# Kernel tuning notes

Measured on AMD Instinct MI355X. Metric: run time of the kernel, lower is better.

Reference implementation:

```python
import jax, jax.numpy as jnp
import numpy as np

D_MODEL = 2048
N_HEADS = 16
N_KV_HEADS = 2
HEAD_DIM = D_MODEL // N_HEADS  # 128
N_REP = N_HEADS // N_KV_HEADS  # 8
SCALE = HEAD_DIM ** -0.5


def setup_inputs() -> dict:
    key = jax.random.key(0)
    ks = jax.random.split(key, 5)
    B, N = 2, 2048
    x = jax.random.normal(ks[0], (B, N, D_MODEL), dtype=jnp.float32)
    # weights stored as [in, out] (math identical to torch Linear x @ W.T)
    s = D_MODEL ** -0.5
    Wq = jax.random.normal(ks[1], (D_MODEL, D_MODEL), dtype=jnp.float32) * s
    Wk = jax.random.normal(ks[2], (D_MODEL, N_KV_HEADS * HEAD_DIM), dtype=jnp.float32) * s
    Wv = jax.random.normal(ks[3], (D_MODEL, N_KV_HEADS * HEAD_DIM), dtype=jnp.float32) * s
    Wo = jax.random.normal(ks[4], (D_MODEL, D_MODEL), dtype=jnp.float32) * s
    return {"x": x, "Wq": Wq, "Wk": Wk, "Wv": Wv, "Wo": Wo}


def reference(x, Wq, Wk, Wv, Wo):
    B, N, C = x.shape
    q = (x @ Wq).reshape(B, N, N_HEADS, HEAD_DIM).transpose(0, 2, 1, 3)      # [B,H,N,hd]
    k = (x @ Wk).reshape(B, N, N_KV_HEADS, HEAD_DIM).transpose(0, 2, 1, 3)   # [B,Hkv,N,hd]
    v = (x @ Wv).reshape(B, N, N_KV_HEADS, HEAD_DIM).transpose(0, 2, 1, 3)
    if N_REP > 1:
        k = jnp.repeat(k, N_REP, axis=1)  # [B,H,N,hd]
        v = jnp.repeat(v, N_REP, axis=1)
    attn = jnp.einsum('bhnd,bhmd->bhnm', q, k) * SCALE
    attn = jax.nn.softmax(attn, axis=-1)
    out = jnp.einsum('bhnm,bhmd->bhnd', attn, v)
    out = out.transpose(0, 2, 1, 3).reshape(B, N, C)
    return out @ Wo
```

## Files before the change

kernel.cpp:

```cpp
#include <hip/hip_runtime.h>

typedef unsigned short u16;
typedef __attribute__((ext_vector_type(4))) float floatx4;
typedef __attribute__((ext_vector_type(2))) float floatx2;
typedef __attribute__((ext_vector_type(8))) __bf16 bf16x8;
typedef __attribute__((ext_vector_type(8))) u16 u16x8;

#define D_MODEL 2048
#define SEQ     2048
#define NH      16
#define NKV     2
#define HD      128
#define QKVN    2560
#define SCALE   0.08838834764831845f
#define QSCALE  (0.08838834764831845f * 1.4426950408889634f)
#define M_STATIC 20.0f

__device__ __forceinline__ u16 f2bf(float f) {
    unsigned int x = __float_as_uint(f);
    return (u16)((x + 0x7fffu + ((x >> 16) & 1u)) >> 16);
}

__device__ __forceinline__ void gload16(const u16* g, u16* l) {
    __builtin_amdgcn_global_load_lds((const __attribute__((address_space(1))) void*)g,
                                     (__attribute__((address_space(3))) void*)l, 16, 0, 0);
}

__global__ void f2b_k(const float* __restrict__ src, u16* __restrict__ dst, long n)
{
    long i = ((long)blockIdx.x * blockDim.x + threadIdx.x) * 8;
    if (i >= n) return;
    float4 a = *(const float4*)(src + i);
    float4 b = *(const float4*)(src + i + 4);
    u16x8 o;
    o[0] = f2bf(a.x); o[1] = f2bf(a.y); o[2] = f2bf(a.z); o[3] = f2bf(a.w);
    o[4] = f2bf(b.x); o[5] = f2bf(b.y); o[6] = f2bf(b.z); o[7] = f2bf(b.w);
    *(u16x8*)(dst + i) = o;
}

struct TrJob { const float* src; u16* dst; int ncol; float scale; };

__global__ void trw_k(TrJob j0, TrJob j1, TrJob j2, TrJob j3)
{
    TrJob j = (blockIdx.z == 0) ? j0 : (blockIdx.z == 1) ? j1
            : (blockIdx.z == 2) ? j2 : j3;
    int c0 = blockIdx.x * 64, r0 = blockIdx.y * 64;
    if (c0 >= j.ncol) return;
    __shared__ float tile[64][65];
    int tx = threadIdx.x, ty = threadIdx.y;
#pragma unroll
    for (int i = 0; i < 8; ++i) {
        int row = ty + i * 8;
        floatx2 v = *(const floatx2*)(j.src + (long)(r0 + row) * j.ncol + c0 + tx * 2);
        tile[row][tx * 2]     = v[0];
        tile[row][tx * 2 + 1] = v[1];
    }
    __syncthreads();
#pragma unroll
    for (int i = 0; i < 8; ++i) {
        int cc = ty + i * 8;
        unsigned int p = (unsigned int)f2bf(tile[tx * 2][cc] * j.scale)
                       | ((unsigned int)f2bf(tile[tx * 2 + 1][cc] * j.scale) << 16);
        *(unsigned int*)(j.dst + (long)(c0 + cc) * 2048 + r0 + tx * 2) = p;
    }
}

__global__ void trv_k(const u16* __restrict__ src, u16* __restrict__ dst)
{
    int b = blockIdx.z;
    const u16* s = src + (long)b * SEQ * QKVN;
    u16* d = dst + (long)b * 256 * 2048;
    int c0 = blockIdx.x * 64, r0 = blockIdx.y * 64;
    __shared__ u16 tile[64][66];
    int tx = threadIdx.x, ty = threadIdx.y;
#pragma unroll
    for (int i = 0; i < 8; ++i) {
        int row = ty + i * 8;
        unsigned int v = *(const unsigned int*)(s + (long)(r0 + row) * QKVN + c0 + tx * 2);
        *(unsigned int*)&tile[row][tx * 2] = v;
    }
    __syncthreads();
#pragma unroll
    for (int i = 0; i < 8; ++i) {
        int cc = ty + i * 8;
        unsigned int p = (unsigned int)tile[tx * 2][cc]
                       | ((unsigned int)tile[tx * 2 + 1][cc] << 16);
        *(unsigned int*)(d + (long)(c0 + cc) * 2048 + r0 + tx * 2) = p;
    }
}

template <bool F32OUT>
__global__ __launch_bounds__(256, 2) void gemm_bt_k(
    const u16* __restrict__ A, const u16* __restrict__ Bt, void* __restrict__ Cv,
    int K, int lda, int ldb, int ldc)
{
    __shared__ __align__(16) u16 As[128 * 64];
    __shared__ __align__(16) u16 Bs[128 * 64];
    const int tid  = threadIdx.x;
    const int wave = tid >> 6, lane = tid & 63;
    const int quad = lane >> 4, l16 = lane & 15;
    const long bm = (long)blockIdx.x * 128;
    const long bn = (long)blockIdx.y * 128;
    const int wr = (wave >> 1) * 64;
    const int wc = (wave & 1) * 64;

    floatx4 acc[4][4] = {};

    for (long k0 = 0; k0 < K; k0 += 64) {
#pragma unroll
        for (int t = 0; t < 4; ++t) {
            int c = tid + t * 256;
            int row = c >> 3, sl = c & 7;
            int kc = sl ^ (row & 7);
            gload16(A + (bm + row) * lda + k0 + kc * 8,
                    As + ((tid & ~63) + t * 256) * 8);
        }
#pragma unroll
        for (int t = 0; t < 4; ++t) {
            int c = tid + t * 256;
            int row = c >> 3, sl = c & 7;
            int kc = sl ^ (row & 7);
            gload16(Bt + (bn + row) * ldb + k0 + kc * 8,
                    Bs + ((tid & ~63) + t * 256) * 8);
        }
        __syncthreads();

#pragma unroll
        for (int ks = 0; ks < 2; ++ks) {
            bf16x8 af[4], bfr[4];
#pragma unroll
            for (int mt = 0; mt < 4; ++mt) {
                int r  = wr + mt * 16 + l16;
                int ch = (ks * 4 + quad) ^ (r & 7);
                af[mt] = *(const bf16x8*)(As + r * 64 + ch * 8);
            }
#pragma unroll
            for (int nt = 0; nt < 4; ++nt) {
                int r  = wc + nt * 16 + l16;
                int ch = (ks * 4 + quad) ^ (r & 7);
                bfr[nt] = *(const bf16x8*)(Bs + r * 64 + ch * 8);
            }
#pragma unroll
            for (int mt = 0; mt < 4; ++mt)
#pragma unroll
                for (int nt = 0; nt < 4; ++nt)
                    acc[mt][nt] = __builtin_amdgcn_mfma_f32_16x16x32_bf16(
                        af[mt], bfr[nt], acc[mt][nt], 0, 0, 0);
        }
        __syncthreads();
    }

#pragma unroll
    for (int mt = 0; mt < 4; ++mt)
#pragma unroll
        for (int nt = 0; nt < 4; ++nt)
#pragma unroll
            for (int r = 0; r < 4; ++r) {
                long row = bm + wr + mt * 16 + quad * 4 + r;
                long col = bn + wc + nt * 16 + l16;
                if (F32OUT) ((float*)Cv)[row * ldc + col] = acc[mt][nt][r];
                else        ((u16*)Cv)[row * ldc + col]   = f2bf(acc[mt][nt][r]);
            }
}

#define KTILE (64 * 128)
#define VTILE (128 * 64)
#define PTILE (256 * 64)
#define NT    (SEQ / 64)

__global__ __launch_bounds__(512, 2) void attn_k(
    const u16* __restrict__ QKV, const u16* __restrict__ Vt, u16* __restrict__ Out)
{
    __shared__ __align__(16) u16 smem[2 * KTILE + 2 * VTILE + 2 * PTILE];

    const int tid  = threadIdx.x;
    const int wave = tid >> 6, lane = tid & 63;
    const int quad = lane >> 4, l16 = lane & 15;
    const int qs = wave & 3;
    const int hf = wave >> 2;
    const int qt = blockIdx.x, h = blockIdx.y, b = blockIdx.z;
    const int kvh = h >> 3;

    const long qrow0 = (long)b * SEQ + (long)qt * 256;
    const u16* Qbase = QKV + qrow0 * QKVN + h * HD;
    const u16* Kbase = QKV + (long)b * SEQ * QKVN + D_MODEL + kvh * HD;
    const u16* Vbase = Vt + ((long)b * NKV + kvh) * (long)HD * SEQ;
    u16* const K0 = smem;
    u16* const K1 = smem + KTILE;
    u16* const V0 = smem + 2 * KTILE;
    u16* const V1 = smem + 2 * KTILE + VTILE;
    u16* const P0 = smem + 2 * KTILE + 2 * VTILE;
    u16* const P1 = P0 + PTILE;

#pragma unroll
    for (int t = 0; t < 8; ++t) {
        int c = tid + t * 512;
        int row = c >> 4, sl = c & 15;
        int dc = sl ^ (row & 15);
        gload16(Qbase + (long)row * QKVN + dc * 8, smem + ((tid & ~63) + t * 512) * 8);
    }
    __syncthreads();

    bf16x8 qa[4][4];
#pragma unroll
    for (int mt = 0; mt < 4; ++mt)
#pragma unroll
        for (int ks = 0; ks < 4; ++ks) {
            int r  = qs * 64 + mt * 16 + l16;
            int ch = (ks * 4 + quad) ^ (r & 15);
            qa[mt][ks] = *(const bf16x8*)(smem + r * 128 + ch * 8);
        }
    __syncthreads();

    floatx4 o[4][4] = {};
    float l_run[4] = { 0.f, 0.f, 0.f, 0.f };
    floatx4 s[4][2];

#pragma unroll
    for (int t = 0; t < 2; ++t) {
        int c = tid + t * 512;
        int row = c >> 4, sl = c & 15;
        int dc = sl ^ (row & 15);
        gload16(Kbase + (long)row * QKVN + dc * 8, K0 + ((tid & ~63) + t * 512) * 8);
    }

    for (int t = 0; t < NT; ++t) {
        __syncthreads();
        u16* const Kc = (t & 1) ? K1 : K0;
        u16* const Ka = (t & 1) ? K0 : K1;
        u16* const Vc = (t & 1) ? V1 : V0;
        u16* const Vp = (t & 1) ? V0 : V1;
        u16* const Pc = (t & 1) ? P1 : P0;
        u16* const Pp = (t & 1) ? P0 : P1;

        if (t + 1 < NT) {
            const long k0n = (long)(t + 1) * 64;
#pragma unroll
            for (int tt = 0; tt < 2; ++tt) {
                int c = tid + tt * 512;
                int row = c >> 4, sl = c & 15;
                int dc = sl ^ (row & 15);
                gload16(Kbase + (k0n + row) * QKVN + dc * 8,
                        Ka + ((tid & ~63) + tt * 512) * 8);
            }
        }
        {
            const long k0v = (long)t * 64;
#pragma unroll
            for (int tt = 0; tt < 2; ++tt) {
                int c = tid + tt * 512;
                int row = c >> 3, sl = c & 7;
                int kc = sl ^ (row & 7);
                gload16(Vbase + (long)row * SEQ + k0v + kc * 8,
                        Vc + ((tid & ~63) + tt * 512) * 8);
            }
        }

        __builtin_amdgcn_s_setprio(1);
#pragma unroll
        for (int mt = 0; mt < 4; ++mt)
#pragma unroll
            for (int nt = 0; nt < 2; ++nt)
                s[mt][nt] = floatx4{0.f, 0.f, 0.f, 0.f};
#pragma unroll
        for (int ks = 0; ks < 4; ++ks) {
            bf16x8 kb[2];
#pragma unroll
            for (int nt = 0; nt < 2; ++nt) {
                int r  = hf * 32 + nt * 16 + l16;
                int ch = (ks * 4 + quad) ^ (r & 15);
                kb[nt] = *(const bf16x8*)(Kc + r * 128 + ch * 8);
            }
#pragma unroll
            for (int mt = 0; mt < 4; ++mt)
#pragma unroll
                for (int nt = 0; nt < 2; ++nt)
                    s[mt][nt] = __builtin_amdgcn_mfma_f32_16x16x32_bf16(
                        kb[nt], qa[mt][ks], s[mt][nt], 0, 0, 0);
        }

        if (t > 0) {
#pragma unroll
            for (int ks = 0; ks < 2; ++ks) {
                bf16x8 pa[4];
#pragma unroll
                for (int mt = 0; mt < 4; ++mt) {
                    int row = qs * 64 + mt * 16 + l16;
                    int chk = (ks * 4 + quad) ^ (row & 7);
                    pa[mt] = *(const bf16x8*)(Pp + row * 64 + chk * 8);
                }
#pragma unroll
                for (int dt = 0; dt < 4; ++dt) {
                    int r  = hf * 64 + dt * 16 + l16;
                    int ch = (ks * 4 + quad) ^ (r & 7);
                    bf16x8 vb = *(const bf16x8*)(Vp + r * 64 + ch * 8);
#pragma unroll
                    for (int mt = 0; mt < 4; ++mt)
                        o[mt][dt] = __builtin_amdgcn_mfma_f32_16x16x32_bf16(
                            pa[mt], vb, o[mt][dt], 0, 0, 0);
                }
            }
        }
        __builtin_amdgcn_s_setprio(0);

#pragma unroll
        for (int mt = 0; mt < 4; ++mt) {
#pragma unroll
            for (int nt = 0; nt < 2; ++nt)
#pragma unroll
                for (int r = 0; r < 4; ++r)
                    s[mt][nt][r] = __builtin_amdgcn_exp2f(s[mt][nt][r] - M_STATIC);
            float ta = (s[mt][0][0] + s[mt][0][1]) + (s[mt][0][2] + s[mt][0][3]);
            float tb = (s[mt][1][0] + s[mt][1][1]) + (s[mt][1][2] + s[mt][1][3]);
            float sum = ta + tb;
            sum += __shfl_xor(sum, 16);
            sum += __shfl_xor(sum, 32);
            l_run[mt] += sum;

            int row = qs * 64 + mt * 16 + l16;
            int m = row & 7;
            u16* base = Pc + row * 64 + (quad & 1) * 4;
#pragma unroll
            for (int nt = 0; nt < 2; ++nt) {
                unsigned int lo, hi;
                asm("v_cvt_pk_bf16_f32 %0, %1, %2"
                    : "=v"(lo) : "v"(s[mt][nt][0]), "v"(s[mt][nt][1]));
                asm("v_cvt_pk_bf16_f32 %0, %1, %2"
                    : "=v"(hi) : "v"(s[mt][nt][2]), "v"(s[mt][nt][3]));
                int chunk = (hf * 4 + nt * 2 + (quad >> 1)) ^ m;
                uint2 val; val.x = lo; val.y = hi;
                *(uint2*)(base + chunk * 8) = val;
            }
        }
    }

    __syncthreads();
    {
        u16* const Pp = ((NT - 1) & 1) ? P1 : P0;
        u16* const Vp = ((NT - 1) & 1) ? V1 : V0;
#pragma unroll
        for (int ks = 0; ks < 2; ++ks) {
            bf16x8 pa[4];
#pragma unroll
            for (int mt = 0; mt < 4; ++mt) {
                int row = qs * 64 + mt * 16 + l16;
                int chk = (ks * 4 + quad) ^ (row & 7);
                pa[mt] = *(const bf16x8*)(Pp + row * 64 + chk * 8);
            }
#pragma unroll
            for (int dt = 0; dt < 4; ++dt) {
                int r  = hf * 64 + dt * 16 + l16;
                int ch = (ks * 4 + quad) ^ (r & 7);
                bf16x8 vb = *(const bf16x8*)(Vp + r * 64 + ch * 8);
#pragma unroll
                for (int mt = 0; mt < 4; ++mt)
                    o[mt][dt] = __builtin_amdgcn_mfma_f32_16x16x32_bf16(
                        pa[mt], vb, o[mt][dt], 0, 0, 0);
            }
        }
    }

    float* lbuf = (float*)K0;
    if (quad == 0) {
#pragma unroll
        for (int mt = 0; mt < 4; ++mt)
            lbuf[(qs * 2 + hf) * 64 + mt * 16 + l16] = l_run[mt];
    }
    __syncthreads();
#pragma unroll
    for (int mt = 0; mt < 4; ++mt)
#pragma unroll
        for (int r = 0; r < 4; ++r) {
            int qq = mt * 16 + quad * 4 + r;
            float lt = lbuf[(qs * 2) * 64 + qq] + lbuf[(qs * 2 + 1) * 64 + qq];
            float inv = 1.f / lt;
            long row = qrow0 + qs * 64 + qq;
#pragma unroll
            for (int dt = 0; dt < 4; ++dt)
                Out[row * D_MODEL + h * HD + hf * 64 + dt * 16 + l16] =
                    f2bf(o[mt][dt][r] * inv);
        }
}

extern "C" void kernel_launch(void* const* d_in, const int* in_sizes, int n_in,
                              void* d_out, int out_size, void* d_ws, size_t ws_size,
                              hipStream_t stream)
{
    const float* X  = (const float*)d_in[0];
    const float* Wq = (const float*)d_in[1];
    const float* Wk = (const float*)d_in[2];
    const float* Wv = (const float*)d_in[3];
    const float* Wo = (const float*)d_in[4];
    float* out = (float*)d_out;

    u16* Xb    = (u16*)d_ws;
    u16* attn  = Xb;
    u16* WtQKV = Xb + (long)4096 * D_MODEL;
    u16* WtO   = WtQKV + (long)QKVN * D_MODEL;
    u16* QKV   = WtO + (long)D_MODEL * D_MODEL;
    u16* Vt    = QKV + (long)4096 * QKVN;

    f2b_k<<<dim3(4096), 256, 0, stream>>>(X, Xb, (long)4096 * D_MODEL);

    TrJob j0 = { Wq, WtQKV,               2048, QSCALE };
    TrJob j1 = { Wk, WtQKV + 2048L * 2048, 256, 1.f };
    TrJob j2 = { Wv, WtQKV + 2304L * 2048, 256, 1.f };
    TrJob j3 = { Wo, WtO,                 2048, 1.f };
    trw_k<<<dim3(32, 32, 4), dim3(32, 8), 0, stream>>>(j0, j1, j2, j3);

    gemm_bt_k<false><<<dim3(32, 20), 256, 0, stream>>>(Xb, WtQKV, QKV, 2048, 2048, 2048, QKVN);

    trv_k<<<dim3(4, 32, 2), dim3(32, 8), 0, stream>>>(QKV + 2304, Vt);

    attn_k<<<dim3(8, NH, 2), 512, 0, stream>>>(QKV, Vt, attn);

    gemm_bt_k<true><<<dim3(32, 16), 256, 0, stream>>>(attn, WtO, out, 2048, 2048, 2048, 2048);
}
```

Before: 282.1 us.

## Load K fragments directly from global into registers, drop K LDS staging

Result: slower. 289.3 us (+2.5%).

```diff
diff --git a/kernel.cpp b/kernel.cpp
--- a/kernel.cpp
+++ b/kernel.cpp
@@ -163,7 +163,6 @@
             }
 }
 
-#define KTILE (64 * 128)
 #define VTILE (128 * 64)
 #define PTILE (256 * 64)
 #define NT    (SEQ / 64)
@@ -171,7 +170,7 @@
 __global__ __launch_bounds__(512, 2) void attn_k(
     const u16* __restrict__ QKV, const u16* __restrict__ Vt, u16* __restrict__ Out)
 {
-    __shared__ __align__(16) u16 smem[2 * KTILE + 2 * VTILE + 2 * PTILE];
+    __shared__ __align__(16) u16 smem[2 * VTILE + 2 * PTILE];
 
     const int tid  = threadIdx.x;
     const int wave = tid >> 6, lane = tid & 63;
@@ -185,11 +184,9 @@
     const u16* Qbase = QKV + qrow0 * QKVN + h * HD;
     const u16* Kbase = QKV + (long)b * SEQ * QKVN + D_MODEL + kvh * HD;
     const u16* Vbase = Vt + ((long)b * NKV + kvh) * (long)HD * SEQ;
-    u16* const K0 = smem;
-    u16* const K1 = smem + KTILE;
-    u16* const V0 = smem + 2 * KTILE;
-    u16* const V1 = smem + 2 * KTILE + VTILE;
-    u16* const P0 = smem + 2 * KTILE + 2 * VTILE;
+    u16* const V0 = smem;
+    u16* const V1 = smem + VTILE;
+    u16* const P0 = smem + 2 * VTILE;
     u16* const P1 = P0 + PTILE;
 
 #pragma unroll
@@ -212,38 +209,27 @@
         }
     __syncthreads();
 
+    const long KADV = 64L * QKVN;
+    const u16* kp0 = Kbase + (long)(hf * 32 + l16) * QKVN + quad * 8;
+    const u16* kp1 = kp0 + 16L * QKVN;
+    bf16x8 kb[2][4];
+#pragma unroll
+    for (int ks = 0; ks < 4; ++ks) {
+        kb[0][ks] = *(const bf16x8*)(kp0 + ks * 32);
+        kb[1][ks] = *(const bf16x8*)(kp1 + ks * 32);
+    }
+
     floatx4 o[4][4] = {};
     float l_run[4] = { 0.f, 0.f, 0.f, 0.f };
     floatx4 s[4][2];
 
-#pragma unroll
-    for (int t = 0; t < 2; ++t) {
-        int c = tid + t * 512;
-        int row = c >> 4, sl = c & 15;
-        int dc = sl ^ (row & 15);
-        gload16(Kbase + (long)row * QKVN + dc * 8, K0 + ((tid & ~63) + t * 512) * 8);
-    }
-
     for (int t = 0; t < NT; ++t) {
         __syncthreads();
-        u16* const Kc = (t & 1) ? K1 : K0;
-        u16* const Ka = (t & 1) ? K0 : K1;
         u16* const Vc = (t & 1) ? V1 : V0;
         u16* const Vp = (t & 1) ? V0 : V1;
         u16* const Pc = (t & 1) ? P1 : P0;
         u16* const Pp = (t & 1) ? P0 : P1;
 
-        if (t + 1 < NT) {
-            const long k0n = (long)(t + 1) * 64;
-#pragma unroll
-            for (int tt = 0; tt < 2; ++tt) {
-                int c = tid + tt * 512;
-                int row = c >> 4, sl = c & 15;
-                int dc = sl ^ (row & 15);
-                gload16(Kbase + (k0n + row) * QKVN + dc * 8,
-                        Ka + ((tid & ~63) + tt * 512) * 8);
-            }
-        }
         {
             const long k0v = (long)t * 64;
 #pragma unroll
@@ -263,20 +249,21 @@
             for (int nt = 0; nt < 2; ++nt)
                 s[mt][nt] = floatx4{0.f, 0.f, 0.f, 0.f};
 #pragma unroll
-        for (int ks = 0; ks < 4; ++ks) {
-            bf16x8 kb[2];
-#pragma unroll
-            for (int nt = 0; nt < 2; ++nt) {
-                int r  = hf * 32 + nt * 16 + l16;
-                int ch = (ks * 4 + quad) ^ (r & 15);
-                kb[nt] = *(const bf16x8*)(Kc + r * 128 + ch * 8);
-            }
+        for (int ks = 0; ks < 4; ++ks)
 #pragma unroll
             for (int mt = 0; mt < 4; ++mt)
 #pragma unroll
                 for (int nt = 0; nt < 2; ++nt)
                     s[mt][nt] = __builtin_amdgcn_mfma_f32_16x16x32_bf16(
-                        kb[nt], qa[mt][ks], s[mt][nt], 0, 0, 0);
+                        kb[nt][ks], qa[mt][ks], s[mt][nt], 0, 0, 0);
+
+        if (t + 1 < NT) {
+            const long adv = (long)(t + 1) * KADV;
+#pragma unroll
+            for (int ks = 0; ks < 4; ++ks) {
+                kb[0][ks] = *(const bf16x8*)(kp0 + adv + ks * 32);
+                kb[1][ks] = *(const bf16x8*)(kp1 + adv + ks * 32);
+            }
         }
 
         if (t > 0) {
@@ -360,7 +347,7 @@
         }
     }
 
-    float* lbuf = (float*)K0;
+    float* lbuf = (float*)V0;
     if (quad == 0) {
 #pragma unroll
         for (int mt = 0; mt < 4; ++mt)
```
